# Optimization experiments

Measured on AMD Instinct MI355X. Metric: run time of the kernel, lower is better.

Reference implementation:

```python
import jax, jax.numpy as jnp
import numpy as np

EPS = 1e-6
ROPE_THETA = 10000.0


def setup_inputs() -> dict:
    key = jax.random.key(0)
    ks = jax.random.split(key, 6)
    B, S, D = 2, 2048, 2048
    H, KVH, HD = 16, 4, 128
    hidden_states = jax.random.normal(ks[0], (B, S, D), dtype=jnp.float32)
    # RoPE tables (HF style: freqs duplicated across the two halves)
    inv_freq = 1.0 / (ROPE_THETA ** (jnp.arange(0, HD, 2, dtype=jnp.float32) / HD))
    pos = jnp.arange(S, dtype=jnp.float32)
    freqs = pos[:, None] * inv_freq[None, :]            # [S, HD/2]
    emb = jnp.concatenate([freqs, freqs], axis=-1)       # [S, HD]
    cos, sin = jnp.cos(emb), jnp.sin(emb)
    w_scale = 0.02
    q_w = jax.random.normal(ks[1], (H * HD, D), dtype=jnp.float32) * w_scale
    k_w = jax.random.normal(ks[2], (KVH * HD, D), dtype=jnp.float32) * w_scale
    v_w = jax.random.normal(ks[3], (KVH * HD, D), dtype=jnp.float32) * w_scale
    o_w = jax.random.normal(ks[4], (D, H * HD), dtype=jnp.float32) * w_scale
    q_norm_w = jnp.ones((HD,), dtype=jnp.float32)
    k_norm_w = jnp.ones((HD,), dtype=jnp.float32)
    return {
        "hidden_states": hidden_states, "cos": cos, "sin": sin,
        "q_w": q_w, "k_w": k_w, "v_w": v_w, "o_w": o_w,
        "q_norm_w": q_norm_w, "k_norm_w": k_norm_w,
    }


def _rms_norm(x, w):
    # Qwen3RMSNorm: fp32 variance, scale, cast back
    xf = x.astype(jnp.float32)
    var = jnp.mean(xf * xf, axis=-1, keepdims=True)
    out = xf * jax.lax.rsqrt(var + EPS)
    return (out * w.astype(jnp.float32)).astype(x.dtype)


def _rotate_half(x):
    half = x.shape[-1] // 2
    return jnp.concatenate([-x[..., half:], x[..., :half]], axis=-1)


def reference(hidden_states, cos, sin, q_w, k_w, v_w, o_w, q_norm_w, k_norm_w):
    B, S, D = hidden_states.shape
    HD = q_norm_w.shape[0]
    H = q_w.shape[0] // HD
    KVH = k_w.shape[0] // HD
    groups = H // KVH
    scale = HD ** -0.5

    # QKV projections (no bias) -> [B, heads, S, HD]
    q = (hidden_states @ q_w.T).reshape(B, S, H, HD)
    k = (hidden_states @ k_w.T).reshape(B, S, KVH, HD)
    v = (hidden_states @ v_w.T).reshape(B, S, KVH, HD)
    q = _rms_norm(q, q_norm_w).transpose(0, 2, 1, 3)   # [B,H,S,HD]
    k = _rms_norm(k, k_norm_w).transpose(0, 2, 1, 3)   # [B,KVH,S,HD]
    v = v.transpose(0, 2, 1, 3)                        # [B,KVH,S,HD]

    # RoPE (broadcast over batch and heads)
    c = cos[None, None, :, :]
    s = sin[None, None, :, :]
    q = q * c + _rotate_half(q) * s
    k = k * c + _rotate_half(k) * s

    # GQA expand kv heads
    if groups > 1:
        k = jnp.repeat(k, groups, axis=1)              # [B,H,S,HD]
        v = jnp.repeat(v, groups, axis=1)

    # SDPA, non-causal, no mask, no dropout
    scores = jnp.einsum("bhqd,bhkd->bhqk", q, k) * scale
    probs = jax.nn.softmax(scores, axis=-1)
    attn = jnp.einsum("bhqk,bhkd->bhqd", probs, v)     # [B,H,S,HD]

    attn = attn.transpose(0, 2, 1, 3).reshape(B, S, H * HD)
    return attn @ o_w.T
```

## Files before the change

kernel.cpp:

```cpp
#include <hip/hip_runtime.h>
#include <hip/hip_bf16.h>
#include <math.h>

#define B_   2
#define S_   2048
#define D_   2048
#define H_   16
#define KVH_ 4
#define HD_  128
#define SCALE 0.08838834764831845f
#define LOG2E 1.44269504088896f
#define EPS_  1e-6f

typedef unsigned short u16;
typedef unsigned int   u32;
typedef __attribute__((ext_vector_type(2)))  unsigned int u32x2;
typedef __attribute__((ext_vector_type(8)))  short bf16x8;
typedef __attribute__((ext_vector_type(4)))  float f32x4;
typedef __attribute__((ext_vector_type(16))) float f32x16;

__device__ __forceinline__ u16 f2bf(float x) {
    union { float f; unsigned int u; } v; v.f = x;
    unsigned int r = v.u + 0x7fffu + ((v.u >> 16) & 1u);
    return (u16)(r >> 16);
}
__device__ __forceinline__ float bf2f(u16 b) {
    union { float f; unsigned int u; } v; v.u = ((unsigned int)b) << 16;
    return v.f;
}
__device__ __forceinline__ u32 cvtpk(float lo, float hi) {
    u32 r;
    asm("v_cvt_pk_bf16_f32 %0, %1, %2" : "=v"(r) : "v"(lo), "v"(hi));
    return r;
}
__device__ __forceinline__ void gload16(const void* g, void* lds) {
    __builtin_amdgcn_global_load_lds(
        (const __attribute__((address_space(1))) unsigned int*)g,
        (__attribute__((address_space(3))) unsigned int*)lds, 16, 0, 0);
}

__global__ __launch_bounds__(256) void f2b_all(
    const float* __restrict__ s0, u16* __restrict__ d0, int n0,
    const float* __restrict__ s1, u16* __restrict__ d1, int n1,
    const float* __restrict__ s2, u16* __restrict__ d2, int n2,
    const float* __restrict__ s3, u16* __restrict__ d3, int n3,
    const float* __restrict__ s4, u16* __restrict__ d4, int n4)
{
    const float* s; u16* d; int n;
    switch (blockIdx.y) {
        case 0: s = s0; d = d0; n = n0; break;
        case 1: s = s1; d = d1; n = n1; break;
        case 2: s = s2; d = d2; n = n2; break;
        case 3: s = s3; d = d3; n = n3; break;
        default: s = s4; d = d4; n = n4; break;
    }
    int i = blockIdx.x * 256 + threadIdx.x;
    if (i >= n) return;
    float4 v = ((const float4*)s)[i];
    ushort4 o = make_ushort4(f2bf(v.x), f2bf(v.y), f2bf(v.z), f2bf(v.w));
    ((ushort4*)d)[i] = o;
}

template<int MODE>
__global__ __launch_bounds__(256) void gemm_bf16(
    const u16* __restrict__ A,
    const u16* __restrict__ Bw,
    u16* __restrict__ Qo, u16* __restrict__ Ko, u16* __restrict__ Vt,
    float* __restrict__ Co)
{
    __shared__ u16 As[128 * 64];
    __shared__ u16 Bs[128 * 64];

    const int t  = threadIdx.x;
    const int w  = t >> 6, l = t & 63;
    const int wm = w >> 1, wn = w & 1;
    const int lr = l & 15, lh = l >> 4;
    const int n0 = blockIdx.x * 128;
    const int m0 = blockIdx.y * 128;

    f32x4 acc[4][4];
    #pragma unroll
    for (int i = 0; i < 4; ++i)
        #pragma unroll
        for (int j = 0; j < 4; ++j)
            acc[i][j] = (f32x4)0.f;

    const int x = (w * 4) * 1024 + l * 16;
    for (int k0 = 0; k0 < 2048; k0 += 64) {
        #pragma unroll
        for (int u = 0; u < 4; ++u) {
            int xb = x + u * 1024;
            int r  = xb >> 7;
            int c  = xb & 127;
            int cs = c ^ ((r & 7) << 4);
            gload16(&A[(size_t)(m0 + r) * 2048 + k0 + (cs >> 1)], &As[(w * 4 + u) * 512]);
            gload16(&Bw[(size_t)(n0 + r) * 2048 + k0 + (cs >> 1)], &Bs[(w * 4 + u) * 512]);
        }
        __syncthreads();
        #pragma unroll
        for (int kc = 0; kc < 2; ++kc) {
            bf16x8 af[4], bfr[4];
            #pragma unroll
            for (int i = 0; i < 4; ++i) {
                int row = wm * 64 + i * 16 + lr;
                int byt = row * 128 + ((kc * 64 + lh * 16) ^ ((row & 7) << 4));
                af[i] = *(const bf16x8*)&As[byt >> 1];
                int rob = wn * 64 + i * 16 + lr;
                int byb = rob * 128 + ((kc * 64 + lh * 16) ^ ((rob & 7) << 4));
                bfr[i] = *(const bf16x8*)&Bs[byb >> 1];
            }
            #pragma unroll
            for (int i = 0; i < 4; ++i)
                #pragma unroll
                for (int j = 0; j < 4; ++j)
                    acc[i][j] = __builtin_amdgcn_mfma_f32_16x16x32_bf16(
                        af[i], bfr[j], acc[i][j], 0, 0, 0);
        }
        __syncthreads();
    }

    #pragma unroll
    for (int i = 0; i < 4; ++i) {
        #pragma unroll
        for (int j = 0; j < 4; ++j) {
            int col = n0 + wn * 64 + j * 16 + lr;
            #pragma unroll
            for (int r = 0; r < 4; ++r) {
                int m = m0 + wm * 64 + i * 16 + lh * 4 + r;
                float v = acc[i][j][r];
                if (MODE == 0) {
                    int bb = m >> 11, s = m & 2047;
                    if (col < 2048) {
                        int hh = col >> 7, d = col & 127;
                        Qo[((size_t)(bb * H_ + hh) * S_ + s) * HD_ + d] = f2bf(v);
                    } else if (col < 2560) {
                        int c2 = col - 2048; int hh = c2 >> 7, d = c2 & 127;
                        Ko[((size_t)(bb * KVH_ + hh) * S_ + s) * HD_ + d] = f2bf(v);
                    } else {
                        int c2 = col - 2560; int hh = c2 >> 7, d = c2 & 127;
                        Vt[((size_t)(bb * KVH_ + hh) * HD_ + d) * S_ + s] = f2bf(v);
                    }
                } else {
                    Co[(size_t)m * 2048 + col] = v;
                }
            }
        }
    }
}

__global__ __launch_bounds__(256) void norm_rope(
    u16* __restrict__ Qb, u16* __restrict__ Kb,
    const float* __restrict__ cosb, const float* __restrict__ sinb,
    const float* __restrict__ qnw, const float* __restrict__ knw)
{
    const int rid = blockIdx.x * 4 + (threadIdx.x >> 6);
    const int l   = threadIdx.x & 63;
    u16* row; const float* wn; int s; float sc;
    if (rid < B_ * H_ * S_) {
        row = Qb + (size_t)rid * HD_; wn = qnw; s = rid & (S_ - 1); sc = SCALE * LOG2E;
    } else {
        int r2 = rid - B_ * H_ * S_;
        row = Kb + (size_t)r2 * HD_; wn = knw; s = r2 & (S_ - 1); sc = 1.f;
    }
    unsigned int u = *(const unsigned int*)&row[2 * l];
    float x0 = bf2f((u16)(u & 0xffff)), x1 = bf2f((u16)(u >> 16));
    float ss = x0 * x0 + x1 * x1;
    #pragma unroll
    for (int off = 1; off < 64; off <<= 1) ss += __shfl_xor(ss, off);
    float rr = rsqrtf(ss * (1.f / 128.f) + 1e-6f);
    float n0 = x0 * rr * wn[2 * l];
    float n1 = x1 * rr * wn[2 * l + 1];
    float p0 = __shfl_xor(n0, 32);
    float p1 = __shfl_xor(n1, 32);
    float sg = (l < 32) ? -1.f : 1.f;
    const float* cp = cosb + s * HD_;
    const float* sp = sinb + s * HD_;
    float o0 = (n0 * cp[2 * l]     + sg * p0 * sp[2 * l])     * sc;
    float o1 = (n1 * cp[2 * l + 1] + sg * p1 * sp[2 * l + 1]) * sc;
    unsigned int o = (unsigned int)f2bf(o0) | ((unsigned int)f2bf(o1) << 16);
    *(unsigned int*)&row[2 * l] = o;
}

__global__ __launch_bounds__(256, 2) void attn_mfma(
    const u16* __restrict__ Q,
    const u16* __restrict__ K,
    const u16* __restrict__ Vt,
    u16* __restrict__ AO)
{
    __shared__ u16 Ks[2][64 * 128];
    __shared__ u16 Vs[2][128 * 64];

    const int t  = threadIdx.x, w = t >> 6, l = t & 63;
    const int lq = l & 31, hi = l >> 5;
    const int id = (blockIdx.x & 7) * 64 + (blockIdx.x >> 3);
    const int qx = id & 15, bh = id >> 4;
    const int bb = bh >> 4, h = bh & 15;
    const int kv = bb * KVH_ + (h >> 2);
    const int q0 = qx * 128 + w * 32;

    const u16* Qp = Q + ((size_t)bh * S_ + q0) * HD_;
    const u16* Kp = K + (size_t)kv * S_ * HD_;
    const u16* Vp = Vt + (size_t)kv * HD_ * S_;

    bf16x8 aq[8];
    #pragma unroll
    for (int ks = 0; ks < 8; ++ks)
        aq[ks] = *(const bf16x8*)&Qp[(size_t)lq * 128 + ks * 16 + hi * 8];

    f32x16 oacc[4];
    #pragma unroll
    for (int dt = 0; dt < 4; ++dt) oacc[dt] = (f32x16)0.f;
    float mrun = -1e30f, lrun = 0.f;

    auto stage = [&](int k0, int buf) {
        #pragma unroll
        for (int u = 0; u < 4; ++u) {
            int xb = (w * 4 + u) * 1024 + l * 16;
            int rk = xb >> 8, ck = xb & 255;
            gload16(&Kp[(size_t)(k0 + rk) * 128 + ((ck ^ ((rk & 7) << 4)) >> 1)],
                    &Ks[buf][(w * 4 + u) * 512]);
            int rv = xb >> 7, cv = xb & 127;
            gload16(&Vp[(size_t)rv * S_ + k0 + ((cv ^ ((rv & 7) << 4)) >> 1)],
                    &Vs[buf][(w * 4 + u) * 512]);
        }
    };

    stage(0, 0);
    __syncthreads();

    const int NT = S_ / 64;
    for (int kt = 0; kt < NT; ++kt) {
        const int cur = kt & 1;
        if (kt + 1 < NT) stage((kt + 1) * 64, cur ^ 1);

        f32x16 sacc[2];
        sacc[0] = (f32x16)0.f; sacc[1] = (f32x16)0.f;
        #pragma unroll
        for (int kb = 0; kb < 2; ++kb) {
            #pragma unroll
            for (int ks = 0; ks < 8; ++ks) {
                int row = kb * 32 + lq;
                int byt = row * 256 + ((ks * 32 + hi * 16) ^ ((row & 7) << 4));
                bf16x8 kf = *(const bf16x8*)&Ks[cur][byt >> 1];
                sacc[kb] = __builtin_amdgcn_mfma_f32_32x32x16_bf16(
                    kf, aq[ks], sacc[kb], 0, 0, 0);
            }
        }

        float mx = -1e30f;
        #pragma unroll
        for (int r = 0; r < 16; ++r)
            mx = fmaxf(mx, fmaxf(sacc[0][r], sacc[1][r]));
        mx = fmaxf(mx, __shfl_xor(mx, 32));
        if (__any(mx > mrun + 8.f)) {
            float mn = fmaxf(mrun, mx);
            float al = __builtin_exp2f(mrun - mn);
            mrun = mn;
            lrun *= al;
            #pragma unroll
            for (int r = 0; r < 16; ++r) {
                int src = (r & 3) + 8 * (r >> 2) + 4 * hi;
                float alr = __shfl(al, src);
                #pragma unroll
                for (int dt = 0; dt < 4; ++dt) oacc[dt][r] *= alr;
            }
        }
        float ps = 0.f;
        #pragma unroll
        for (int kb = 0; kb < 2; ++kb)
            #pragma unroll
            for (int r = 0; r < 16; ++r) {
                float p = __builtin_exp2f(sacc[kb][r] - mrun);
                sacc[kb][r] = p;
                ps += p;
            }
        ps += __shfl_xor(ps, 32);
        lrun += ps;

        #pragma unroll
        for (int kb = 0; kb < 2; ++kb) {
            u32 wv[8];
            #pragma unroll
            for (int i = 0; i < 8; ++i)
                wv[i] = cvtpk(sacc[kb][2 * i], sacc[kb][2 * i + 1]);
            #pragma unroll
            for (int k2 = 0; k2 < 2; ++k2) {
                u32x2 r0 = __builtin_amdgcn_permlane32_swap(
                    wv[4 * k2 + 0], wv[4 * k2 + 2], false, false);
                u32x2 r1 = __builtin_amdgcn_permlane32_swap(
                    wv[4 * k2 + 1], wv[4 * k2 + 3], false, false);
                union { u32 u[4]; bf16x8 v; } pa;
                pa.u[0] = r0.x; pa.u[1] = r1.x;
                pa.u[2] = r0.y; pa.u[3] = r1.y;
                int kloc = (kb * 2 + k2) * 16 + hi * 8;
                #pragma unroll
                for (int dt = 0; dt < 4; ++dt) {
                    int rowv = dt * 32 + lq;
                    int byv  = rowv * 128 + ((kloc * 2) ^ ((rowv & 7) << 4));
                    bf16x8 vf = *(const bf16x8*)&Vs[cur][byv >> 1];
                    oacc[dt] = __builtin_amdgcn_mfma_f32_32x32x16_bf16(
                        pa.v, vf, oacc[dt], 0, 0, 0);
                }
            }
        }
        __syncthreads();
    }

    #pragma unroll
    for (int r = 0; r < 16; ++r) {
        int src = (r & 3) + 8 * (r >> 2) + 4 * hi;
        float linv = 1.f / __shfl(lrun, src);
        int s = q0 + src;
        size_t base = ((size_t)bb * S_ + s) * 2048 + h * 128 + lq;
        #pragma unroll
        for (int dt = 0; dt < 4; ++dt)
            AO[base + dt * 32] = f2bf(oacc[dt][r] * linv);
    }
}

extern "C" void kernel_launch(void* const* d_in, const int* in_sizes, int n_in,
                              void* d_out, int out_size, void* d_ws, size_t ws_size,
                              hipStream_t stream) {
    (void)in_sizes; (void)n_in; (void)out_size; (void)ws_size;
    const float* hid  = (const float*)d_in[0];
    const float* cosb = (const float*)d_in[1];
    const float* sinb = (const float*)d_in[2];
    const float* qw   = (const float*)d_in[3];
    const float* kw   = (const float*)d_in[4];
    const float* vw   = (const float*)d_in[5];
    const float* ow   = (const float*)d_in[6];
    const float* qnw  = (const float*)d_in[7];
    const float* knw  = (const float*)d_in[8];

    u16* ws   = (u16*)d_ws;
    u16* hidB = ws;
    u16* Wc   = ws + 8388608;
    u16* owB  = ws + 14680064;
    u16* Qb   = ws + 18874368;
    u16* Kb   = ws + 27262976;
    u16* VtB  = ws + 29360128;
    u16* AO   = ws + 31457280;

    f2b_all<<<dim3(8192, 5), 256, 0, stream>>>(
        hid, hidB, 2097152,
        qw,  Wc,            1048576,
        kw,  Wc + 4194304,  262144,
        vw,  Wc + 5242880,  262144,
        ow,  owB,           1048576);

    gemm_bf16<0><<<dim3(24, 32), 256, 0, stream>>>(hidB, Wc, Qb, Kb, VtB, nullptr);
    norm_rope<<<20480, 256, 0, stream>>>(Qb, Kb, cosb, sinb, qnw, knw);
    attn_mfma<<<512, 256, 0, stream>>>(Qb, Kb, VtB, AO);
    gemm_bf16<1><<<dim3(16, 32), 256, 0, stream>>>(AO, owB, nullptr, nullptr, nullptr,
                                                   (float*)d_out);
}
```

Measured before the change: 237.0 us.

## Defer PV MFMA by one tile to overlap with softmax

Software-pipelines the attention loop. The packed bf16 probabilities of each KV tile are kept in registers, and their P·V MFMAs are issued during the next iteration, after the QK^T MFMAs and before the softmax. This lets matrix-core work overlap the exp and reduction math of the current tile. V tiles move to a triple-buffered LDS ring so the previous tile stays valid while the next one streams in. The cost is extra register pressure (16 more u32 per thread) and 16 KB more LDS, which could hurt occupancy.

```diff
diff --git a/kernel.cpp b/kernel.cpp
--- a/kernel.cpp
+++ b/kernel.cpp
@@ -188,7 +188,7 @@
     u16* __restrict__ AO)
 {
     __shared__ u16 Ks[2][64 * 128];
-    __shared__ u16 Vs[2][128 * 64];
+    __shared__ u16 Vs[3][128 * 64];
 
     const int t  = threadIdx.x, w = t >> 6, l = t & 63;
     const int lq = l & 31, hi = l >> 5;
@@ -211,27 +211,28 @@
     #pragma unroll
     for (int dt = 0; dt < 4; ++dt) oacc[dt] = (f32x16)0.f;
     float mrun = -1e30f, lrun = 0.f;
-
-    auto stage = [&](int k0, int buf) {
+    u32 pan[16];
+
+    auto stage = [&](int k0, int kbuf, int vbuf) {
         #pragma unroll
         for (int u = 0; u < 4; ++u) {
             int xb = (w * 4 + u) * 1024 + l * 16;
             int rk = xb >> 8, ck = xb & 255;
             gload16(&Kp[(size_t)(k0 + rk) * 128 + ((ck ^ ((rk & 7) << 4)) >> 1)],
-                    &Ks[buf][(w * 4 + u) * 512]);
+                    &Ks[kbuf][(w * 4 + u) * 512]);
             int rv = xb >> 7, cv = xb & 127;
             gload16(&Vp[(size_t)rv * S_ + k0 + ((cv ^ ((rv & 7) << 4)) >> 1)],
-                    &Vs[buf][(w * 4 + u) * 512]);
+                    &Vs[vbuf][(w * 4 + u) * 512]);
         }
     };
 
-    stage(0, 0);
+    stage(0, 0, 0);
     __syncthreads();
 
     const int NT = S_ / 64;
     for (int kt = 0; kt < NT; ++kt) {
-        const int cur = kt & 1;
-        if (kt + 1 < NT) stage((kt + 1) * 64, cur ^ 1);
+        const int kcur = kt & 1;
+        if (kt + 1 < NT) stage((kt + 1) * 64, (kt + 1) & 1, (kt + 1) % 3);
 
         f32x16 sacc[2];
         sacc[0] = (f32x16)0.f; sacc[1] = (f32x16)0.f;
@@ -241,7 +242,7 @@
             for (int ks = 0; ks < 8; ++ks) {
                 int row = kb * 32 + lq;
                 int byt = row * 256 + ((ks * 32 + hi * 16) ^ ((row & 7) << 4));
-                bf16x8 kf = *(const bf16x8*)&Ks[cur][byt >> 1];
+                bf16x8 kf = *(const bf16x8*)&Ks[kcur][byt >> 1];
                 sacc[kb] = __builtin_amdgcn_mfma_f32_32x32x16_bf16(
                     kf, aq[ks], sacc[kb], 0, 0, 0);
             }
@@ -252,6 +253,26 @@
         for (int r = 0; r < 16; ++r)
             mx = fmaxf(mx, fmaxf(sacc[0][r], sacc[1][r]));
         mx = fmaxf(mx, __shfl_xor(mx, 32));
+
+        if (kt > 0) {
+            const int vprev = (kt + 2) % 3;
+            #pragma unroll
+            for (int g = 0; g < 4; ++g) {
+                union { u32 u[4]; bf16x8 v; } pa;
+                pa.u[0] = pan[g * 4 + 0]; pa.u[1] = pan[g * 4 + 1];
+                pa.u[2] = pan[g * 4 + 2]; pa.u[3] = pan[g * 4 + 3];
+                int kloc = g * 16 + hi * 8;
+                #pragma unroll
+                for (int dt = 0; dt < 4; ++dt) {
+                    int rowv = dt * 32 + lq;
+                    int byv  = rowv * 128 + ((kloc * 2) ^ ((rowv & 7) << 4));
+                    bf16x8 vf = *(const bf16x8*)&Vs[vprev][byv >> 1];
+                    oacc[dt] = __builtin_amdgcn_mfma_f32_32x32x16_bf16(
+                        pa.v, vf, oacc[dt], 0, 0, 0);
+                }
+            }
+        }
+
         if (__any(mx > mrun + 8.f)) {
             float mn = fmaxf(mrun, mx);
             float al = __builtin_exp2f(mrun - mn);
@@ -265,6 +286,7 @@
                 for (int dt = 0; dt < 4; ++dt) oacc[dt][r] *= alr;
             }
         }
+
         float ps = 0.f;
         #pragma unroll
         for (int kb = 0; kb < 2; ++kb)
@@ -289,21 +311,31 @@
                     wv[4 * k2 + 0], wv[4 * k2 + 2], false, false);
                 u32x2 r1 = __builtin_amdgcn_permlane32_swap(
                     wv[4 * k2 + 1], wv[4 * k2 + 3], false, false);
-                union { u32 u[4]; bf16x8 v; } pa;
-                pa.u[0] = r0.x; pa.u[1] = r1.x;
-                pa.u[2] = r0.y; pa.u[3] = r1.y;
-                int kloc = (kb * 2 + k2) * 16 + hi * 8;
-                #pragma unroll
-                for (int dt = 0; dt < 4; ++dt) {
-                    int rowv = dt * 32 + lq;
-                    int byv  = rowv * 128 + ((kloc * 2) ^ ((rowv & 7) << 4));
-                    bf16x8 vf = *(const bf16x8*)&Vs[cur][byv >> 1];
-                    oacc[dt] = __builtin_amdgcn_mfma_f32_32x32x16_bf16(
-                        pa.v, vf, oacc[dt], 0, 0, 0);
-                }
+                int g = kb * 2 + k2;
+                pan[g * 4 + 0] = r0.x; pan[g * 4 + 1] = r1.x;
+                pan[g * 4 + 2] = r0.y; pan[g * 4 + 3] = r1.y;
             }
         }
         __syncthreads();
+    }
+
+    {
+        const int vprev = (NT - 1) % 3;
+        #pragma unroll
+        for (int g = 0; g < 4; ++g) {
+            union { u32 u[4]; bf16x8 v; } pa;
+            pa.u[0] = pan[g * 4 + 0]; pa.u[1] = pan[g * 4 + 1];
+            pa.u[2] = pan[g * 4 + 2]; pa.u[3] = pan[g * 4 + 3];
+            int kloc = g * 16 + hi * 8;
+            #pragma unroll
+            for (int dt = 0; dt < 4; ++dt) {
+                int rowv = dt * 32 + lq;
+                int byv  = rowv * 128 + ((kloc * 2) ^ ((rowv & 7) << 4));
+                bf16x8 vf = *(const bf16x8*)&Vs[vprev][byv >> 1];
+                oacc[dt] = __builtin_amdgcn_mfma_f32_32x32x16_bf16(
+                    pa.v, vf, oacc[dt], 0, 0, 0);
+            }
+        }
     }
 
     #pragma unroll
```

New measurement: 233.6 us. Within noise of the previous version (-1.4%).

## Split attention over KV halves with separate combine kernel for more blocks

Applied to the files above, without the earlier changes.

Attention is split along the key dimension into two halves, so the launch doubles to 1024 blocks. The KV tile shrinks to 32 keys, which cuts LDS use and allows 4 blocks per CU. Each split writes unnormalized partial outputs plus running max and sum, and a new combine kernel merges them into AO. It also uses packed subtract/add and max3 instructions in the softmax. The cost is extra global traffic for the partial outputs, one more kernel launch, and partials rounded to bf16 before they are combined.

```diff
diff --git a/kernel.cpp b/kernel.cpp
--- a/kernel.cpp
+++ b/kernel.cpp
@@ -10,11 +10,13 @@
 #define HD_  128
 #define SCALE 0.08838834764831845f
 #define LOG2E 1.44269504088896f
+#define QSC_  (SCALE * LOG2E)
 #define EPS_  1e-6f
 
 typedef unsigned short u16;
 typedef unsigned int   u32;
 typedef __attribute__((ext_vector_type(2)))  unsigned int u32x2;
+typedef __attribute__((ext_vector_type(2)))  float f32x2;
 typedef __attribute__((ext_vector_type(8)))  short bf16x8;
 typedef __attribute__((ext_vector_type(4)))  float f32x4;
 typedef __attribute__((ext_vector_type(16))) float f32x16;
@@ -32,6 +34,17 @@
     u32 r;
     asm("v_cvt_pk_bf16_f32 %0, %1, %2" : "=v"(r) : "v"(lo), "v"(hi));
     return r;
+}
+__device__ __forceinline__ f32x2 pk_sub(f32x2 a, f32x2 b) {
+    f32x2 r;
+    asm("v_pk_add_f32 %0, %1, %2 neg_lo:[0,1] neg_hi:[0,1]" : "=v"(r) : "v"(a), "v"(b));
+    return r;
+}
+__device__ __forceinline__ f32x2 pk_add(f32x2 a, f32x2 b) {
+    f32x2 r; asm("v_pk_add_f32 %0, %1, %2" : "=v"(r) : "v"(a), "v"(b)); return r;
+}
+__device__ __forceinline__ float max3f(float a, float b, float c) {
+    float r; asm("v_max3_f32 %0, %1, %2, %3" : "=v"(r) : "v"(a), "v"(b), "v"(c)); return r;
 }
 __device__ __forceinline__ void gload16(const void* g, void* lds) {
     __builtin_amdgcn_global_load_lds(
@@ -157,7 +170,7 @@
     const int l   = threadIdx.x & 63;
     u16* row; const float* wn; int s; float sc;
     if (rid < B_ * H_ * S_) {
-        row = Qb + (size_t)rid * HD_; wn = qnw; s = rid & (S_ - 1); sc = SCALE * LOG2E;
+        row = Qb + (size_t)rid * HD_; wn = qnw; s = rid & (S_ - 1); sc = QSC_;
     } else {
         int r2 = rid - B_ * H_ * S_;
         row = Kb + (size_t)r2 * HD_; wn = knw; s = r2 & (S_ - 1); sc = 1.f;
@@ -167,7 +180,7 @@
     float ss = x0 * x0 + x1 * x1;
     #pragma unroll
     for (int off = 1; off < 64; off <<= 1) ss += __shfl_xor(ss, off);
-    float rr = rsqrtf(ss * (1.f / 128.f) + 1e-6f);
+    float rr = rsqrtf(ss * (1.f / 128.f) + EPS_);
     float n0 = x0 * rr * wn[2 * l];
     float n1 = x1 * rr * wn[2 * l + 1];
     float p0 = __shfl_xor(n0, 32);
@@ -181,26 +194,32 @@
     *(unsigned int*)&row[2 * l] = o;
 }
 
-__global__ __launch_bounds__(256, 2) void attn_mfma(
+__global__ __launch_bounds__(256, 4) void attn_split(
     const u16* __restrict__ Q,
     const u16* __restrict__ K,
     const u16* __restrict__ Vt,
-    u16* __restrict__ AO)
+    u16* __restrict__ Op0,
+    u16* __restrict__ Op1,
+    float2* __restrict__ Ml)
 {
-    __shared__ u16 Ks[2][64 * 128];
-    __shared__ u16 Vs[2][128 * 64];
+    __shared__ u16 Ks[2][32 * 128];
+    __shared__ u16 Vs[2][128 * 32];
 
     const int t  = threadIdx.x, w = t >> 6, l = t & 63;
     const int lq = l & 31, hi = l >> 5;
-    const int id = (blockIdx.x & 7) * 64 + (blockIdx.x >> 3);
-    const int qx = id & 15, bh = id >> 4;
+    const int id = ((int)blockIdx.x & 7) * 128 + ((int)blockIdx.x >> 3);
+    const int split = id & 1;
+    const int qx = (id >> 1) & 15;
+    const int bh = id >> 5;
     const int bb = bh >> 4, h = bh & 15;
     const int kv = bb * KVH_ + (h >> 2);
     const int q0 = qx * 128 + w * 32;
+    const int kbase = split * (S_ / 2);
 
     const u16* Qp = Q + ((size_t)bh * S_ + q0) * HD_;
     const u16* Kp = K + (size_t)kv * S_ * HD_;
     const u16* Vp = Vt + (size_t)kv * HD_ * S_;
+    u16* Op = split ? Op1 : Op0;
 
     bf16x8 aq[8];
     #pragma unroll
@@ -214,44 +233,43 @@
 
     auto stage = [&](int k0, int buf) {
         #pragma unroll
-        for (int u = 0; u < 4; ++u) {
-            int xb = (w * 4 + u) * 1024 + l * 16;
+        for (int u = 0; u < 2; ++u) {
+            int xb = (w * 2 + u) * 1024 + l * 16;
             int rk = xb >> 8, ck = xb & 255;
             gload16(&Kp[(size_t)(k0 + rk) * 128 + ((ck ^ ((rk & 7) << 4)) >> 1)],
-                    &Ks[buf][(w * 4 + u) * 512]);
-            int rv = xb >> 7, cv = xb & 127;
-            gload16(&Vp[(size_t)rv * S_ + k0 + ((cv ^ ((rv & 7) << 4)) >> 1)],
-                    &Vs[buf][(w * 4 + u) * 512]);
+                    &Ks[buf][(w * 2 + u) * 512]);
+            int rv = xb >> 6, cv = xb & 63;
+            gload16(&Vp[(size_t)rv * S_ + k0 + ((cv ^ ((rv & 3) << 4)) >> 1)],
+                    &Vs[buf][(w * 2 + u) * 512]);
         }
     };
 
-    stage(0, 0);
+    stage(kbase, 0);
     __syncthreads();
 
-    const int NT = S_ / 64;
+    const int NT = (S_ / 2) / 32;
     for (int kt = 0; kt < NT; ++kt) {
         const int cur = kt & 1;
-        if (kt + 1 < NT) stage((kt + 1) * 64, cur ^ 1);
-
-        f32x16 sacc[2];
-        sacc[0] = (f32x16)0.f; sacc[1] = (f32x16)0.f;
-        #pragma unroll
-        for (int kb = 0; kb < 2; ++kb) {
-            #pragma unroll
-            for (int ks = 0; ks < 8; ++ks) {
-                int row = kb * 32 + lq;
-                int byt = row * 256 + ((ks * 32 + hi * 16) ^ ((row & 7) << 4));
-                bf16x8 kf = *(const bf16x8*)&Ks[cur][byt >> 1];
-                sacc[kb] = __builtin_amdgcn_mfma_f32_32x32x16_bf16(
-                    kf, aq[ks], sacc[kb], 0, 0, 0);
-            }
-        }
-
-        float mx = -1e30f;
-        #pragma unroll
-        for (int r = 0; r < 16; ++r)
-            mx = fmaxf(mx, fmaxf(sacc[0][r], sacc[1][r]));
-        mx = fmaxf(mx, __shfl_xor(mx, 32));
+        if (kt + 1 < NT) stage(kbase + (kt + 1) * 32, cur ^ 1);
+
+        f32x16 sacc = (f32x16)0.f;
+        #pragma unroll
+        for (int ks = 0; ks < 8; ++ks) {
+            int byt = lq * 256 + ((ks * 32 + hi * 16) ^ ((lq & 7) << 4));
+            bf16x8 kf = *(const bf16x8*)&Ks[cur][byt >> 1];
+            sacc = __builtin_amdgcn_mfma_f32_32x32x16_bf16(kf, aq[ks], sacc, 0, 0, 0);
+        }
+
+        float mxa = max3f(sacc[0], sacc[1], sacc[2]);
+        mxa = max3f(mxa, sacc[3], sacc[4]);
+        mxa = max3f(mxa, sacc[5], sacc[6]);
+        float mxb = max3f(sacc[7], sacc[8], sacc[9]);
+        mxb = max3f(mxb, sacc[10], sacc[11]);
+        mxb = max3f(mxb, sacc[12], sacc[13]);
+        float mx = max3f(mxa, sacc[14], sacc[15]);
+        mx = max3f(mx, mxb, __shfl_xor(mx, 32));
+        mx = fmaxf(mx, __shfl_xor(mxb, 32));
+
         if (__any(mx > mrun + 8.f)) {
             float mn = fmaxf(mrun, mx);
             float al = __builtin_exp2f(mrun - mn);
@@ -265,42 +283,45 @@
                 for (int dt = 0; dt < 4; ++dt) oacc[dt][r] *= alr;
             }
         }
-        float ps = 0.f;
-        #pragma unroll
-        for (int kb = 0; kb < 2; ++kb)
-            #pragma unroll
-            for (int r = 0; r < 16; ++r) {
-                float p = __builtin_exp2f(sacc[kb][r] - mrun);
-                sacc[kb][r] = p;
-                ps += p;
+
+        f32x2 mr2; mr2.x = mrun; mr2.y = mrun;
+        f32x2 ps2; ps2.x = 0.f; ps2.y = 0.f;
+        {
+            f32x2* s2 = (f32x2*)&sacc;
+            #pragma unroll
+            for (int i = 0; i < 8; ++i) {
+                f32x2 dv = pk_sub(s2[i], mr2);
+                dv.x = __builtin_exp2f(dv.x);
+                dv.y = __builtin_exp2f(dv.y);
+                s2[i] = dv;
+                ps2 = pk_add(ps2, dv);
             }
+        }
+        float ps = ps2.x + ps2.y;
         ps += __shfl_xor(ps, 32);
         lrun += ps;
 
-        #pragma unroll
-        for (int kb = 0; kb < 2; ++kb) {
-            u32 wv[8];
-            #pragma unroll
-            for (int i = 0; i < 8; ++i)
-                wv[i] = cvtpk(sacc[kb][2 * i], sacc[kb][2 * i + 1]);
-            #pragma unroll
-            for (int k2 = 0; k2 < 2; ++k2) {
-                u32x2 r0 = __builtin_amdgcn_permlane32_swap(
-                    wv[4 * k2 + 0], wv[4 * k2 + 2], false, false);
-                u32x2 r1 = __builtin_amdgcn_permlane32_swap(
-                    wv[4 * k2 + 1], wv[4 * k2 + 3], false, false);
-                union { u32 u[4]; bf16x8 v; } pa;
-                pa.u[0] = r0.x; pa.u[1] = r1.x;
-                pa.u[2] = r0.y; pa.u[3] = r1.y;
-                int kloc = (kb * 2 + k2) * 16 + hi * 8;
-                #pragma unroll
-                for (int dt = 0; dt < 4; ++dt) {
-                    int rowv = dt * 32 + lq;
-                    int byv  = rowv * 128 + ((kloc * 2) ^ ((rowv & 7) << 4));
-                    bf16x8 vf = *(const bf16x8*)&Vs[cur][byv >> 1];
-                    oacc[dt] = __builtin_amdgcn_mfma_f32_32x32x16_bf16(
-                        pa.v, vf, oacc[dt], 0, 0, 0);
-                }
+        u32 wv[8];
+        #pragma unroll
+        for (int i = 0; i < 8; ++i)
+            wv[i] = cvtpk(sacc[2 * i], sacc[2 * i + 1]);
+        #pragma unroll
+        for (int k2 = 0; k2 < 2; ++k2) {
+            u32x2 r0 = __builtin_amdgcn_permlane32_swap(
+                wv[4 * k2 + 0], wv[4 * k2 + 2], false, false);
+            u32x2 r1 = __builtin_amdgcn_permlane32_swap(
+                wv[4 * k2 + 1], wv[4 * k2 + 3], false, false);
+            union { u32 u[4]; bf16x8 v; } pa;
+            pa.u[0] = r0.x; pa.u[1] = r1.x;
+            pa.u[2] = r0.y; pa.u[3] = r1.y;
+            int kloc = k2 * 16 + hi * 8;
+            #pragma unroll
+            for (int dt = 0; dt < 4; ++dt) {
+                int rowv = dt * 32 + lq;
+                int byv  = rowv * 64 + ((kloc * 2) ^ ((rowv & 3) << 4));
+                bf16x8 vf = *(const bf16x8*)&Vs[cur][byv >> 1];
+                oacc[dt] = __builtin_amdgcn_mfma_f32_32x32x16_bf16(
+                    pa.v, vf, oacc[dt], 0, 0, 0);
             }
         }
         __syncthreads();
@@ -309,13 +330,37 @@
     #pragma unroll
     for (int r = 0; r < 16; ++r) {
         int src = (r & 3) + 8 * (r >> 2) + 4 * hi;
-        float linv = 1.f / __shfl(lrun, src);
-        int s = q0 + src;
-        size_t base = ((size_t)bb * S_ + s) * 2048 + h * 128 + lq;
+        size_t base = ((size_t)bh * S_ + q0 + src) * 128 + lq;
         #pragma unroll
         for (int dt = 0; dt < 4; ++dt)
-            AO[base + dt * 32] = f2bf(oacc[dt][r] * linv);
-    }
+            Op[base + dt * 32] = f2bf(oacc[dt][r]);
+    }
+    if (l < 32) {
+        float2 ml; ml.x = mrun; ml.y = lrun;
+        Ml[(size_t)split * (B_ * H_ * S_) + (size_t)bh * S_ + q0 + l] = ml;
+    }
+}
+
+__global__ __launch_bounds__(256) void combine_split(
+    const u16* __restrict__ Op0, const u16* __restrict__ Op1,
+    const float2* __restrict__ Ml, u16* __restrict__ AO)
+{
+    const int rid = blockIdx.x * 4 + (threadIdx.x >> 6);
+    const int l   = threadIdx.x & 63;
+    float2 ml0 = Ml[rid];
+    float2 ml1 = Ml[B_ * H_ * S_ + rid];
+    float m  = fmaxf(ml0.x, ml1.x);
+    float w0 = __builtin_exp2f(ml0.x - m);
+    float w1 = __builtin_exp2f(ml1.x - m);
+    float inv = 1.f / (w0 * ml0.y + w1 * ml1.y);
+    u32 a = *(const u32*)&Op0[(size_t)rid * 128 + 2 * l];
+    u32 b = *(const u32*)&Op1[(size_t)rid * 128 + 2 * l];
+    float o0 = (w0 * bf2f((u16)(a & 0xffff)) + w1 * bf2f((u16)(b & 0xffff))) * inv;
+    float o1 = (w0 * bf2f((u16)(a >> 16))    + w1 * bf2f((u16)(b >> 16)))    * inv;
+    int bh = rid >> 11, s = rid & 2047;
+    int bb = bh >> 4, h = bh & 15;
+    u32 o = (u32)f2bf(o0) | ((u32)f2bf(o1) << 16);
+    *(u32*)&AO[((size_t)(bb * S_ + s)) * 2048 + h * 128 + 2 * l] = o;
 }
 
 extern "C" void kernel_launch(void* const* d_in, const int* in_sizes, int n_in,
@@ -340,6 +385,9 @@
     u16* Kb   = ws + 27262976;
     u16* VtB  = ws + 29360128;
     u16* AO   = ws + 31457280;
+    u16* Op1  = ws + 39845888;
+    float2* Ml = (float2*)(ws + 48234496);
+    u16* Op0  = hidB;
 
     f2b_all<<<dim3(8192, 5), 256, 0, stream>>>(
         hid, hidB, 2097152,
@@ -350,7 +398,8 @@
 
     gemm_bf16<0><<<dim3(24, 32), 256, 0, stream>>>(hidB, Wc, Qb, Kb, VtB, nullptr);
     norm_rope<<<20480, 256, 0, stream>>>(Qb, Kb, cosb, sinb, qnw, knw);
-    attn_mfma<<<512, 256, 0, stream>>>(Qb, Kb, VtB, AO);
+    attn_split<<<1024, 256, 0, stream>>>(Qb, Kb, VtB, Op0, Op1, Ml);
+    combine_split<<<16384, 256, 0, stream>>>(Op0, Op1, Ml, AO);
     gemm_bf16<1><<<dim3(16, 32), 256, 0, stream>>>(AO, owB, nullptr, nullptr, nullptr,
                                                    (float*)d_out);
 }
```

Result: slower. 339.6 us (+43.3%).
